# Kernel optimization log

Measured on AMD Instinct MI355X. Metric: run time of the kernel, lower is better.

## Reference

```python
import jax, jax.numpy as jnp
import numpy as np

N_NODES = 100000
N_EDGES = 6400000
F_IN, F_HID, F_OUT = 5, 5, 10


def setup_inputs() -> dict:
    key = jax.random.key(0)
    ks = jax.random.split(key, 9)
    x = jax.random.normal(ks[0], (N_NODES, F_IN), dtype=jnp.float32)
    src = jax.random.randint(ks[1], (N_EDGES,), 0, N_NODES, dtype=jnp.int32)
    dst = jax.random.randint(ks[2], (N_EDGES,), 0, N_NODES, dtype=jnp.int32)
    s1 = 1.0 / np.sqrt(F_IN)
    s2 = 1.0 / np.sqrt(F_HID)
    W_self1 = jax.random.uniform(ks[3], (F_IN, F_HID), jnp.float32, -s1, s1)
    W_neigh1 = jax.random.uniform(ks[4], (F_IN, F_HID), jnp.float32, -s1, s1)
    b1 = jnp.zeros((F_HID,), jnp.float32)
    W_self2 = jax.random.uniform(ks[5], (F_HID, F_OUT), jnp.float32, -s2, s2)
    W_neigh2 = jax.random.uniform(ks[6], (F_HID, F_OUT), jnp.float32, -s2, s2)
    b2 = jnp.zeros((F_OUT,), jnp.float32)
    return {"x": x, "src": src, "dst": dst,
            "W_self1": W_self1, "W_neigh1": W_neigh1, "b1": b1,
            "W_self2": W_self2, "W_neigh2": W_neigh2, "b2": b2}


def _sage_mean(h, src, dst, W_self, W_neigh, b):
    # DGL SAGEConv (mean): out = h @ W_self + mean_{u->v}(h_u) @ W_neigh + b
    msg = h[src]                                        # [E, F] gather
    agg = jax.ops.segment_sum(msg, dst, num_segments=N_NODES)   # [N, F]
    deg = jax.ops.segment_sum(jnp.ones((src.shape[0],), h.dtype), dst,
                              num_segments=N_NODES)     # [N]
    h_neigh = agg / jnp.maximum(deg, 1.0)[:, None]
    return h @ W_self + h_neigh @ W_neigh + b


def reference(x, src, dst, W_self1, W_neigh1, b1, W_self2, W_neigh2, b2):
    h = jax.nn.sigmoid(_sage_mean(x, src, dst, W_self1, W_neigh1, b1))
    out = jax.nn.sigmoid(_sage_mean(h, src, dst, W_self2, W_neigh2, b2))
    return out
```

## Files before the change

kernel.cpp:

```cpp
#include <hip/hip_runtime.h>
#include <hip/hip_fp16.h>
#include <math.h>


#define F_IN  5
#define F_HID 5
#define F_OUT 10

#define NBSHIFT 7
#define NPB     (1 << NBSHIFT)
#define PBLK    1024
#define CHUNK   8192
#define EPT     8
#define BSTRIDE 9216
#define SBLK    512
#define SPT     18
#define LPN2    8
#define LBLK    256

__device__ __forceinline__ float sigmoidf(float v) {
    return 1.0f / (1.0f + __expf(-v));
}

__global__ void partition(const float* __restrict__ x,
                          const int* __restrict__ src, const int* __restrict__ dst,
                          int* __restrict__ bcursor, int* __restrict__ packed,
                          uint4* __restrict__ xh, int E, int N, int NB) {
    __shared__ int cnt[PBLK], excl[PBLK], adj[PBLK];
    __shared__ int wsum[16];
    __shared__ int buf[CHUNK];
    __shared__ unsigned char dlow[CHUNK];
    int t = threadIdx.x;
    int lane = t & 63, w = t >> 6;
    if (t < NPB) {
        int v = (blockIdx.x << NBSHIFT) + t;
        if (v < N) {
            const float* xr = x + (size_t)v * 5;
            float4 a = *(const float4*)xr;
            float a4 = xr[4];
            uint4 o;
            o.x = (unsigned)__half_as_ushort(__float2half_rn(a.x)) |
                  ((unsigned)__half_as_ushort(__float2half_rn(a.y)) << 16);
            o.y = (unsigned)__half_as_ushort(__float2half_rn(a.z)) |
                  ((unsigned)__half_as_ushort(__float2half_rn(a.w)) << 16);
            o.z = (unsigned)__half_as_ushort(__float2half_rn(a4));
            o.w = 0;
            xh[v] = o;
        }
    }
    cnt[t] = 0;
    __syncthreads();
    int base = blockIdx.x * CHUNK;
    int end  = min(base + CHUNK, E);
    int sarr[EPT], darr[EPT];
    #pragma unroll
    for (int r = 0; r < 2; ++r) {
        int i = base + r * 4096 + t * 4;
        if (i + 4 <= end) {
            int4 sv = *(const int4*)(src + i);
            int4 dv = *(const int4*)(dst + i);
            sarr[r*4+0]=sv.x; sarr[r*4+1]=sv.y; sarr[r*4+2]=sv.z; sarr[r*4+3]=sv.w;
            darr[r*4+0]=dv.x; darr[r*4+1]=dv.y; darr[r*4+2]=dv.z; darr[r*4+3]=dv.w;
        } else {
            #pragma unroll
            for (int c = 0; c < 4; ++c) {
                int i2 = i + c;
                if (i2 < end) { sarr[r*4+c] = src[i2]; darr[r*4+c] = dst[i2]; }
            }
        }
    }
    int esd[EPT];
    int ebp[EPT];
    #pragma unroll
    for (int j = 0; j < EPT; ++j) {
        int i = base + (j >> 2) * 4096 + t * 4 + (j & 3);
        if (i < end) {
            int sv = sarr[j], d = darr[j];
            int b  = d >> NBSHIFT;
            int p  = atomicAdd(&cnt[b], 1);
            esd[j] = sv | ((d & (NPB - 1)) << 17);
            ebp[j] = (b << 14) | p;
        }
    }
    __syncthreads();
    int v = cnt[t];
    int incl = v;
    #pragma unroll
    for (int off = 1; off < 64; off <<= 1) {
        int u = __shfl_up(incl, off, 64);
        if (lane >= off) incl += u;
    }
    if (lane == 63) wsum[w] = incl;
    __syncthreads();
    if (t < 16) {
        int s = wsum[t];
        #pragma unroll
        for (int off = 1; off < 16; off <<= 1) {
            int u = __shfl_up(s, off, 16);
            if (t >= off) s += u;
        }
        wsum[t] = s;
    }
    __syncthreads();
    int wbase = (w > 0) ? wsum[w - 1] : 0;
    excl[t] = incl - v + wbase;
    __syncthreads();
    if (t < NB) {
        int cb = cnt[t];
        int go = cb ? atomicAdd(&bcursor[t], cb) : 0;
        adj[t] = t * BSTRIDE + go - excl[t];
    }
    __syncthreads();
    #pragma unroll
    for (int j = 0; j < EPT; ++j) {
        int i = base + (j >> 2) * 4096 + t * 4 + (j & 3);
        if (i < end) {
            int b   = ebp[j] >> 14;
            int pos = excl[b] + (ebp[j] & 0x3FFF);
            buf[pos]  = (esd[j] & 0x1FFFF) | (b << 17);
            dlow[pos] = (unsigned char)(esd[j] >> 17);
        }
    }
    __syncthreads();
    int cval = end - base;
    for (int p = t; p < cval; p += PBLK) {
        int e = buf[p];
        int b = e >> 17;
        packed[adj[b] + p] = (e & 0x1FFFF) | ((int)dlow[p] << 17);
    }
}

__global__ void __launch_bounds__(SBLK, 8)
sortagg1(const uint4* __restrict__ xh, int* __restrict__ packed,
         const int* __restrict__ bcursor,
         const float* __restrict__ Ws, const float* __restrict__ Wn,
         const float* __restrict__ bias,
         uint4* __restrict__ hp, int2* __restrict__ sd, int N) {
    __shared__ int buf[BSTRIDE];
    __shared__ int ncnt[NPB], nst[NPB];
    __shared__ int w0sum;
    int b = blockIdx.x, t = threadIdx.x;
    int s0  = b * BSTRIDE;
    int cnt = min(bcursor[b], BSTRIDE);
    if (t < NPB) ncnt[t] = 0;
    __syncthreads();
    int myv[SPT];
    #pragma unroll
    for (int r = 0; r < 4; ++r) {
        int i = r * 2048 + t * 4;
        if (i + 4 <= cnt) {
            int4 q = *(const int4*)(packed + s0 + i);
            myv[r*4+0]=q.x; myv[r*4+1]=q.y; myv[r*4+2]=q.z; myv[r*4+3]=q.w;
        } else {
            #pragma unroll
            for (int c = 0; c < 4; ++c) {
                int i2 = i + c;
                myv[r*4+c] = (i2 < cnt) ? packed[s0 + i2] : 0;
            }
        }
    }
    {
        int i = 8192 + t * 2;
        if (i + 2 <= cnt) {
            int2 q = *(const int2*)(packed + s0 + i);
            myv[16] = q.x; myv[17] = q.y;
        } else {
            myv[16] = (i     < cnt) ? packed[s0 + i]     : 0;
            myv[17] = (i + 1 < cnt) ? packed[s0 + i + 1] : 0;
        }
    }
    short myp[SPT];
    #pragma unroll
    for (int j = 0; j < SPT; ++j) {
        int i = (j < 16) ? ((j >> 2) * 2048 + t * 4 + (j & 3)) : (8192 + t * 2 + (j - 16));
        if (i < cnt) {
            myp[j] = (short)atomicAdd(&ncnt[(myv[j] >> 17) & (NPB - 1)], 1);
        }
    }
    __syncthreads();
    if (t < NPB) {
        int lane = t & 63;
        int vv = ncnt[t];
        int incl = vv;
        #pragma unroll
        for (int off = 1; off < 64; off <<= 1) {
            int u = __shfl_up(incl, off, 64);
            if (lane >= off) incl += u;
        }
        if (t == 63) w0sum = incl;
        nst[t] = incl - vv;
    }
    __syncthreads();
    if (t >= 64 && t < NPB) nst[t] += w0sum;
    __syncthreads();
    if (t < NPB) {
        int node = (b << NBSHIFT) + t;
        if (node < N) sd[node] = make_int2(s0 + nst[t], ncnt[t]);
    }
    __syncthreads();
    #pragma unroll
    for (int j = 0; j < SPT; ++j) {
        int i = (j < 16) ? ((j >> 2) * 2048 + t * 4 + (j & 3)) : (8192 + t * 2 + (j - 16));
        if (i < cnt) {
            int e = myv[j];
            buf[nst[(e >> 17) & (NPB - 1)] + (int)myp[j]] = e;
        }
    }
    __syncthreads();
    for (int i = t; i < cnt; i += SBLK)
        packed[s0 + i] = buf[i] & 0x1FFFF;
    int sub = t & 3, ln = t >> 2;
    int node = (b << NBSHIFT) + ln;
    float a0 = 0, a1 = 0, a2 = 0, a3 = 0, a4 = 0;
    int dg = 0;
    if (node < N) {
        int st = nst[ln];
        dg = ncnt[ln];
        for (int k = sub; k < dg; k += 4) {
            int u = buf[st + k] & 0x1FFFF;
            uint4 q = xh[u];
            float2 f01 = __half22float2(*(const __half2*)&q.x);
            float2 f23 = __half22float2(*(const __half2*)&q.y);
            float2 f45 = __half22float2(*(const __half2*)&q.z);
            a0 += f01.x; a1 += f01.y; a2 += f23.x; a3 += f23.y; a4 += f45.x;
        }
    }
    #pragma unroll
    for (int off = 2; off > 0; off >>= 1) {
        a0 += __shfl_down(a0, off, 4);
        a1 += __shfl_down(a1, off, 4);
        a2 += __shfl_down(a2, off, 4);
        a3 += __shfl_down(a3, off, 4);
        a4 += __shfl_down(a4, off, 4);
    }
    if (sub != 0 || node >= N) return;
    float rd = 1.0f / fmaxf((float)dg, 1.0f);
    float ni[F_IN] = { a0 * rd, a1 * rd, a2 * rd, a3 * rd, a4 * rd };
    uint4 qs = xh[node];
    float2 s01 = __half22float2(*(const __half2*)&qs.x);
    float2 s23 = __half22float2(*(const __half2*)&qs.y);
    float2 s45 = __half22float2(*(const __half2*)&qs.z);
    float xi[F_IN] = { s01.x, s01.y, s23.x, s23.y, s45.x };
    unsigned short hu[5];
    #pragma unroll
    for (int j = 0; j < F_HID; ++j) {
        float acc = bias[j];
        #pragma unroll
        for (int f = 0; f < F_IN; ++f)
            acc += xi[f] * Ws[f * F_HID + j] + ni[f] * Wn[f * F_HID + j];
        hu[j] = __half_as_ushort(__float2half_rn(sigmoidf(acc)));
    }
    uint4 o;
    o.x = (unsigned)hu[0] | ((unsigned)hu[1] << 16);
    o.y = (unsigned)hu[2] | ((unsigned)hu[3] << 16);
    o.z = (unsigned)hu[4];
    o.w = 0;
    hp[node] = o;
}

__global__ void layer2(const uint4* __restrict__ hp, const int* __restrict__ eidx,
                       const int2* __restrict__ sd,
                       const float* __restrict__ Ws, const float* __restrict__ Wn,
                       const float* __restrict__ b,
                       float* __restrict__ out, int N) {
    int tid = blockIdx.x * blockDim.x + threadIdx.x;
    int v   = tid >> 3;
    int sub = threadIdx.x & (LPN2 - 1);
    if (v >= N) return;
    int2 sdv = sd[v];
    int st = sdv.x, dg = sdv.y;
    int len = (dg + LPN2 - 1) >> 3;
    int k0 = sub * len;
    int k1 = min(k0 + len, dg);
    float s0 = 0, s1 = 0, s2 = 0, s3 = 0, s4 = 0;
    int k = k0;
    for (; k + 4 <= k1; k += 4) {
        int4 qi;
        __builtin_memcpy(&qi, eidx + st + k, 16);
        #pragma unroll
        for (int c = 0; c < 4; ++c) {
            int u = (c == 0) ? qi.x : (c == 1) ? qi.y : (c == 2) ? qi.z : qi.w;
            uint4 q = hp[u];
            float2 f01 = __half22float2(*(const __half2*)&q.x);
            float2 f23 = __half22float2(*(const __half2*)&q.y);
            float2 f45 = __half22float2(*(const __half2*)&q.z);
            s0 += f01.x; s1 += f01.y; s2 += f23.x; s3 += f23.y; s4 += f45.x;
        }
    }
    for (; k < k1; ++k) {
        int u = eidx[st + k];
        uint4 q = hp[u];
        float2 f01 = __half22float2(*(const __half2*)&q.x);
        float2 f23 = __half22float2(*(const __half2*)&q.y);
        float2 f45 = __half22float2(*(const __half2*)&q.z);
        s0 += f01.x; s1 += f01.y; s2 += f23.x; s3 += f23.y; s4 += f45.x;
    }
    #pragma unroll
    for (int off = LPN2 / 2; off > 0; off >>= 1) {
        s0 += __shfl_down(s0, off, LPN2);
        s1 += __shfl_down(s1, off, LPN2);
        s2 += __shfl_down(s2, off, LPN2);
        s3 += __shfl_down(s3, off, LPN2);
        s4 += __shfl_down(s4, off, LPN2);
    }
    if (sub != 0) return;
    float rd = 1.0f / fmaxf((float)dg, 1.0f);
    float ni[F_HID] = { s0 * rd, s1 * rd, s2 * rd, s3 * rd, s4 * rd };
    uint4 q = hp[v];
    float2 f01 = __half22float2(*(const __half2*)&q.x);
    float2 f23 = __half22float2(*(const __half2*)&q.y);
    float2 f45 = __half22float2(*(const __half2*)&q.z);
    float hi[F_HID] = { f01.x, f01.y, f23.x, f23.y, f45.x };
    #pragma unroll
    for (int j = 0; j < F_OUT; ++j) {
        float acc = b[j];
        #pragma unroll
        for (int f = 0; f < F_HID; ++f)
            acc += hi[f] * Ws[f * F_OUT + j] + ni[f] * Wn[f * F_OUT + j];
        out[(size_t)v * F_OUT + j] = sigmoidf(acc);
    }
}

extern "C" void kernel_launch(void* const* d_in, const int* in_sizes, int n_in,
                              void* d_out, int out_size, void* d_ws, size_t ws_size,
                              hipStream_t stream) {
    const float* x   = (const float*)d_in[0];
    const int*   src = (const int*)d_in[1];
    const int*   dst = (const int*)d_in[2];
    const float* Ws1 = (const float*)d_in[3];
    const float* Wn1 = (const float*)d_in[4];
    const float* b1  = (const float*)d_in[5];
    const float* Ws2 = (const float*)d_in[6];
    const float* Wn2 = (const float*)d_in[7];
    const float* b2  = (const float*)d_in[8];
    float* out = (float*)d_out;

    const int N  = in_sizes[0] / F_IN;
    const int E  = in_sizes[1];
    const int NB = (N + NPB - 1) >> NBSHIFT;

    int*   bcursor = (int*)d_ws;
    uint4* xh      = (uint4*)(bcursor + 1024);
    int2*  sd      = (int2*)(xh + N);
    int*   packed  = (int*)(sd + N);
    uint4* hp      = (uint4*)(packed + (size_t)NB * BSTRIDE);

    const int ablocks = (E + CHUNK - 1) / CHUNK;
    const int lgrid   = ((size_t)N * LPN2 + LBLK - 1) / LBLK;

    (void)hipMemsetAsync(bcursor, 0, 1024 * sizeof(int), stream);
    partition<<<ablocks, PBLK, 0, stream>>>(x, src, dst, bcursor, packed, xh, E, N, NB);
    sortagg1<<<NB, SBLK, 0, stream>>>(xh, packed, bcursor, Ws1, Wn1, b1, hp, sd, N);
    layer2<<<lgrid, LBLK, 0, stream>>>(hp, packed, sd, Ws2, Wn2, b2, out, N);
}
```

Before: 200.1 us.

## Fuse partition, sort-aggregate and layer-2 into one cooperative persistent kernel

```diff
diff --git a/kernel.cpp b/kernel.cpp
--- a/kernel.cpp
+++ b/kernel.cpp
@@ -1,6 +1,9 @@
 #include <hip/hip_runtime.h>
 #include <hip/hip_fp16.h>
+#include <hip/hip_cooperative_groups.h>
 #include <math.h>
+
+namespace cg = cooperative_groups;
 
 
 #define F_IN  5
@@ -17,9 +20,341 @@
 #define SPT     18
 #define LPN2    8
 #define LBLK    256
+#define FBLK    512
+#define EPTF    16
 
 __device__ __forceinline__ float sigmoidf(float v) {
     return 1.0f / (1.0f + __expf(-v));
+}
+
+__device__ __forceinline__ uint4 pack_h5(const float* __restrict__ xr) {
+    float4 a = *(const float4*)xr;
+    float a4 = xr[4];
+    uint4 o;
+    o.x = (unsigned)__half_as_ushort(__float2half_rn(a.x)) |
+          ((unsigned)__half_as_ushort(__float2half_rn(a.y)) << 16);
+    o.y = (unsigned)__half_as_ushort(__float2half_rn(a.z)) |
+          ((unsigned)__half_as_ushort(__float2half_rn(a.w)) << 16);
+    o.z = (unsigned)__half_as_ushort(__float2half_rn(a4));
+    o.w = 0;
+    return o;
+}
+
+union SharedU {
+    struct {
+        int cnt[1024];
+        int excl[1024];
+        int adj[1024];
+        int wsum[16];
+        int buf[CHUNK];
+        unsigned char dlow[CHUNK];
+    } part;
+    struct {
+        int buf[BSTRIDE];
+        int ncnt[NPB];
+        int nst[NPB];
+        int w0sum;
+    } srt;
+};
+
+__global__ void __launch_bounds__(FBLK, 4)
+fused(const float* __restrict__ x,
+      const int* __restrict__ src, const int* __restrict__ dst,
+      int* __restrict__ bcursor, int* __restrict__ packed,
+      uint4* __restrict__ xh,
+      const float* __restrict__ Ws1, const float* __restrict__ Wn1,
+      const float* __restrict__ b1,
+      uint4* __restrict__ hp, int2* __restrict__ sd,
+      const float* __restrict__ Ws2, const float* __restrict__ Wn2,
+      const float* __restrict__ b2,
+      float* __restrict__ out,
+      int E, int N, int NB, int NCHUNK, int NG2) {
+    __shared__ SharedU sh;
+    cg::grid_group gg = cg::this_grid();
+    int t = threadIdx.x;
+    int lane = t & 63, w = t >> 6;
+
+    if (blockIdx.x == 0) { bcursor[t] = 0; bcursor[t + FBLK] = 0; }
+    __threadfence();
+    gg.sync();
+    __threadfence();
+
+    for (int cc = blockIdx.x; cc < NCHUNK; cc += gridDim.x) {
+        int base = cc * CHUNK;
+        int end  = min(base + CHUNK, E);
+        sh.part.cnt[t] = 0;
+        sh.part.cnt[t + FBLK] = 0;
+        if (t < NPB) {
+            int v = (cc << NBSHIFT) + t;
+            if (v < N) xh[v] = pack_h5(x + (size_t)v * 5);
+        }
+        __syncthreads();
+        int sarr[EPTF], darr[EPTF];
+        #pragma unroll
+        for (int r = 0; r < 4; ++r) {
+            int i = base + r * 2048 + t * 4;
+            if (i + 4 <= end) {
+                int4 sv = *(const int4*)(src + i);
+                int4 dv = *(const int4*)(dst + i);
+                sarr[r*4+0]=sv.x; sarr[r*4+1]=sv.y; sarr[r*4+2]=sv.z; sarr[r*4+3]=sv.w;
+                darr[r*4+0]=dv.x; darr[r*4+1]=dv.y; darr[r*4+2]=dv.z; darr[r*4+3]=dv.w;
+            } else {
+                #pragma unroll
+                for (int c = 0; c < 4; ++c) {
+                    int i2 = i + c;
+                    if (i2 < end) { sarr[r*4+c] = src[i2]; darr[r*4+c] = dst[i2]; }
+                }
+            }
+        }
+        #pragma unroll
+        for (int j = 0; j < EPTF; ++j) {
+            int i = base + (j >> 2) * 2048 + t * 4 + (j & 3);
+            if (i < end) {
+                int d = darr[j];
+                int b = d >> NBSHIFT;
+                int p = atomicAdd(&sh.part.cnt[b], 1);
+                sarr[j] |= (d & (NPB - 1)) << 17;
+                darr[j] = (b << 14) | p;
+            }
+        }
+        __syncthreads();
+        int c0 = sh.part.cnt[2 * t], c1 = sh.part.cnt[2 * t + 1];
+        int s = c0 + c1;
+        int incl = s;
+        #pragma unroll
+        for (int off = 1; off < 64; off <<= 1) {
+            int u = __shfl_up(incl, off, 64);
+            if (lane >= off) incl += u;
+        }
+        if (lane == 63) sh.part.wsum[w] = incl;
+        __syncthreads();
+        if (t < 8) {
+            int sv = sh.part.wsum[t];
+            #pragma unroll
+            for (int off = 1; off < 8; off <<= 1) {
+                int u = __shfl_up(sv, off, 8);
+                if (t >= off) sv += u;
+            }
+            sh.part.wsum[t] = sv;
+        }
+        __syncthreads();
+        int wbase = (w > 0) ? sh.part.wsum[w - 1] : 0;
+        int e0 = incl - s + wbase;
+        sh.part.excl[2 * t]     = e0;
+        sh.part.excl[2 * t + 1] = e0 + c0;
+        __syncthreads();
+        for (int bb = t; bb < NB; bb += FBLK) {
+            int cb = sh.part.cnt[bb];
+            int go = cb ? atomicAdd(&bcursor[bb], cb) : 0;
+            sh.part.adj[bb] = bb * BSTRIDE + go - sh.part.excl[bb];
+        }
+        __syncthreads();
+        #pragma unroll
+        for (int j = 0; j < EPTF; ++j) {
+            int i = base + (j >> 2) * 2048 + t * 4 + (j & 3);
+            if (i < end) {
+                int b   = darr[j] >> 14;
+                int pos = sh.part.excl[b] + (darr[j] & 0x3FFF);
+                sh.part.buf[pos]  = (sarr[j] & 0x1FFFF) | (b << 17);
+                sh.part.dlow[pos] = (unsigned char)(sarr[j] >> 17);
+            }
+        }
+        __syncthreads();
+        int cval = end - base;
+        for (int p = t; p < cval; p += FBLK) {
+            int e = sh.part.buf[p];
+            int b = e >> 17;
+            packed[sh.part.adj[b] + p] = (e & 0x1FFFF) | ((int)sh.part.dlow[p] << 17);
+        }
+        __syncthreads();
+    }
+    __threadfence();
+    gg.sync();
+    __threadfence();
+
+    for (int bb = blockIdx.x; bb < NB; bb += gridDim.x) {
+        int sb   = bb * BSTRIDE;
+        int cntb = min(bcursor[bb], BSTRIDE);
+        if (t < NPB) sh.srt.ncnt[t] = 0;
+        __syncthreads();
+        int myv[SPT];
+        #pragma unroll
+        for (int r = 0; r < 4; ++r) {
+            int i = r * 2048 + t * 4;
+            if (i + 4 <= cntb) {
+                int4 q = *(const int4*)(packed + sb + i);
+                myv[r*4+0]=q.x; myv[r*4+1]=q.y; myv[r*4+2]=q.z; myv[r*4+3]=q.w;
+            } else {
+                #pragma unroll
+                for (int c = 0; c < 4; ++c) {
+                    int i2 = i + c;
+                    myv[r*4+c] = (i2 < cntb) ? packed[sb + i2] : 0;
+                }
+            }
+        }
+        {
+            int i = 8192 + t * 2;
+            if (i + 2 <= cntb) {
+                int2 q = *(const int2*)(packed + sb + i);
+                myv[16] = q.x; myv[17] = q.y;
+            } else {
+                myv[16] = (i     < cntb) ? packed[sb + i]     : 0;
+                myv[17] = (i + 1 < cntb) ? packed[sb + i + 1] : 0;
+            }
+        }
+        short myp[SPT];
+        #pragma unroll
+        for (int j = 0; j < SPT; ++j) {
+            int i = (j < 16) ? ((j >> 2) * 2048 + t * 4 + (j & 3)) : (8192 + t * 2 + (j - 16));
+            if (i < cntb) {
+                myp[j] = (short)atomicAdd(&sh.srt.ncnt[(myv[j] >> 17) & (NPB - 1)], 1);
+            }
+        }
+        __syncthreads();
+        if (t < NPB) {
+            int vv = sh.srt.ncnt[t];
+            int incl = vv;
+            #pragma unroll
+            for (int off = 1; off < 64; off <<= 1) {
+                int u = __shfl_up(incl, off, 64);
+                if ((t & 63) >= off) incl += u;
+            }
+            if (t == 63) sh.srt.w0sum = incl;
+            sh.srt.nst[t] = incl - vv;
+        }
+        __syncthreads();
+        if (t >= 64 && t < NPB) sh.srt.nst[t] += sh.srt.w0sum;
+        __syncthreads();
+        if (t < NPB) {
+            int node = (bb << NBSHIFT) + t;
+            if (node < N) sd[node] = make_int2(sb + sh.srt.nst[t], sh.srt.ncnt[t]);
+        }
+        __syncthreads();
+        #pragma unroll
+        for (int j = 0; j < SPT; ++j) {
+            int i = (j < 16) ? ((j >> 2) * 2048 + t * 4 + (j & 3)) : (8192 + t * 2 + (j - 16));
+            if (i < cntb) {
+                int e = myv[j];
+                sh.srt.buf[sh.srt.nst[(e >> 17) & (NPB - 1)] + (int)myp[j]] = e;
+            }
+        }
+        __syncthreads();
+        for (int i = t; i < cntb; i += FBLK)
+            packed[sb + i] = sh.srt.buf[i] & 0x1FFFF;
+        int sub = t & 3, ln = t >> 2;
+        int node = (bb << NBSHIFT) + ln;
+        float a0 = 0, a1 = 0, a2 = 0, a3 = 0, a4 = 0;
+        int dg = 0;
+        if (node < N) {
+            int st = sh.srt.nst[ln];
+            dg = sh.srt.ncnt[ln];
+            for (int k = sub; k < dg; k += 4) {
+                int u = sh.srt.buf[st + k] & 0x1FFFF;
+                uint4 q = xh[u];
+                float2 f01 = __half22float2(*(const __half2*)&q.x);
+                float2 f23 = __half22float2(*(const __half2*)&q.y);
+                float2 f45 = __half22float2(*(const __half2*)&q.z);
+                a0 += f01.x; a1 += f01.y; a2 += f23.x; a3 += f23.y; a4 += f45.x;
+            }
+        }
+        #pragma unroll
+        for (int off = 2; off > 0; off >>= 1) {
+            a0 += __shfl_down(a0, off, 4);
+            a1 += __shfl_down(a1, off, 4);
+            a2 += __shfl_down(a2, off, 4);
+            a3 += __shfl_down(a3, off, 4);
+            a4 += __shfl_down(a4, off, 4);
+        }
+        if (sub == 0 && node < N) {
+            float rd = 1.0f / fmaxf((float)dg, 1.0f);
+            float ni[F_IN] = { a0 * rd, a1 * rd, a2 * rd, a3 * rd, a4 * rd };
+            uint4 qs = xh[node];
+            float2 s01 = __half22float2(*(const __half2*)&qs.x);
+            float2 s23 = __half22float2(*(const __half2*)&qs.y);
+            float2 s45 = __half22float2(*(const __half2*)&qs.z);
+            float xi[F_IN] = { s01.x, s01.y, s23.x, s23.y, s45.x };
+            unsigned short hu[5];
+            #pragma unroll
+            for (int j = 0; j < F_HID; ++j) {
+                float acc = b1[j];
+                #pragma unroll
+                for (int f = 0; f < F_IN; ++f)
+                    acc += xi[f] * Ws1[f * F_HID + j] + ni[f] * Wn1[f * F_HID + j];
+                hu[j] = __half_as_ushort(__float2half_rn(sigmoidf(acc)));
+            }
+            uint4 o;
+            o.x = (unsigned)hu[0] | ((unsigned)hu[1] << 16);
+            o.y = (unsigned)hu[2] | ((unsigned)hu[3] << 16);
+            o.z = (unsigned)hu[4];
+            o.w = 0;
+            hp[node] = o;
+        }
+        __syncthreads();
+    }
+    __threadfence();
+    gg.sync();
+    __threadfence();
+
+    for (int g = blockIdx.x; g < NG2; g += gridDim.x) {
+        int v   = (g << 6) + (t >> 3);
+        int sub = t & (LPN2 - 1);
+        float s0 = 0, s1 = 0, s2 = 0, s3 = 0, s4 = 0;
+        int stv = 0, dg = 0;
+        if (v < N) {
+            int2 sdv = sd[v];
+            stv = sdv.x; dg = sdv.y;
+        }
+        int len = (dg + LPN2 - 1) >> 3;
+        int k0 = sub * len;
+        int k1 = min(k0 + len, dg);
+        int k = k0;
+        for (; k + 4 <= k1; k += 4) {
+            int4 qi;
+            __builtin_memcpy(&qi, packed + stv + k, 16);
+            #pragma unroll
+            for (int c = 0; c < 4; ++c) {
+                int u = (c == 0) ? qi.x : (c == 1) ? qi.y : (c == 2) ? qi.z : qi.w;
+                uint4 q = hp[u];
+                float2 f01 = __half22float2(*(const __half2*)&q.x);
+                float2 f23 = __half22float2(*(const __half2*)&q.y);
+                float2 f45 = __half22float2(*(const __half2*)&q.z);
+                s0 += f01.x; s1 += f01.y; s2 += f23.x; s3 += f23.y; s4 += f45.x;
+            }
+        }
+        for (; k < k1; ++k) {
+            int u = packed[stv + k];
+            uint4 q = hp[u];
+            float2 f01 = __half22float2(*(const __half2*)&q.x);
+            float2 f23 = __half22float2(*(const __half2*)&q.y);
+            float2 f45 = __half22float2(*(const __half2*)&q.z);
+            s0 += f01.x; s1 += f01.y; s2 += f23.x; s3 += f23.y; s4 += f45.x;
+        }
+        #pragma unroll
+        for (int off = LPN2 / 2; off > 0; off >>= 1) {
+            s0 += __shfl_down(s0, off, LPN2);
+            s1 += __shfl_down(s1, off, LPN2);
+            s2 += __shfl_down(s2, off, LPN2);
+            s3 += __shfl_down(s3, off, LPN2);
+            s4 += __shfl_down(s4, off, LPN2);
+        }
+        if (sub == 0 && v < N) {
+            float rd = 1.0f / fmaxf((float)dg, 1.0f);
+            float ni[F_HID] = { s0 * rd, s1 * rd, s2 * rd, s3 * rd, s4 * rd };
+            uint4 q = hp[v];
+            float2 f01 = __half22float2(*(const __half2*)&q.x);
+            float2 f23 = __half22float2(*(const __half2*)&q.y);
+            float2 f45 = __half22float2(*(const __half2*)&q.z);
+            float hi[F_HID] = { f01.x, f01.y, f23.x, f23.y, f45.x };
+            #pragma unroll
+            for (int j = 0; j < F_OUT; ++j) {
+                float acc = b2[j];
+                #pragma unroll
+                for (int f = 0; f < F_HID; ++f)
+                    acc += hi[f] * Ws2[f * F_OUT + j] + ni[f] * Wn2[f * F_OUT + j];
+                out[(size_t)v * F_OUT + j] = sigmoidf(acc);
+            }
+        }
+    }
 }
 
 __global__ void partition(const float* __restrict__ x,
@@ -34,19 +369,7 @@
     int lane = t & 63, w = t >> 6;
     if (t < NPB) {
         int v = (blockIdx.x << NBSHIFT) + t;
-        if (v < N) {
-            const float* xr = x + (size_t)v * 5;
-            float4 a = *(const float4*)xr;
-            float a4 = xr[4];
-            uint4 o;
-            o.x = (unsigned)__half_as_ushort(__float2half_rn(a.x)) |
-                  ((unsigned)__half_as_ushort(__float2half_rn(a.y)) << 16);
-            o.y = (unsigned)__half_as_ushort(__float2half_rn(a.z)) |
-                  ((unsigned)__half_as_ushort(__float2half_rn(a.w)) << 16);
-            o.z = (unsigned)__half_as_ushort(__float2half_rn(a4));
-            o.w = 0;
-            xh[v] = o;
-        }
+        if (v < N) xh[v] = pack_h5(x + (size_t)v * 5);
     }
     cnt[t] = 0;
     __syncthreads();
@@ -69,8 +392,7 @@
             }
         }
     }
-    int esd[EPT];
-    int ebp[EPT];
+    int esd[EPT], ebp[EPT];
     #pragma unroll
     for (int j = 0; j < EPT; ++j) {
         int i = base + (j >> 2) * 4096 + t * 4 + (j & 3);
@@ -338,6 +660,8 @@
     const int N  = in_sizes[0] / F_IN;
     const int E  = in_sizes[1];
     const int NB = (N + NPB - 1) >> NBSHIFT;
+    const int NCHUNK = (E + CHUNK - 1) / CHUNK;
+    const int NG2 = (N + 63) >> 6;
 
     int*   bcursor = (int*)d_ws;
     uint4* xh      = (uint4*)(bcursor + 1024);
@@ -345,6 +669,32 @@
     int*   packed  = (int*)(sd + N);
     uint4* hp      = (uint4*)(packed + (size_t)NB * BSTRIDE);
 
+    static int coop_blocks = -2;
+    if (coop_blocks == -2) {
+        int dev = 0; (void)hipGetDevice(&dev);
+        int can = 0, ncu = 0, bpc = 0;
+        (void)hipDeviceGetAttribute(&can, hipDeviceAttributeCooperativeLaunch, dev);
+        (void)hipDeviceGetAttribute(&ncu, hipDeviceAttributeMultiprocessorCount, dev);
+        hipError_t oe = hipOccupancyMaxActiveBlocksPerMultiprocessor(&bpc, fused, FBLK, 0);
+        coop_blocks = (can && ncu > 0 && oe == hipSuccess && bpc > 0) ? bpc * ncu : 0;
+    }
+
+    if (coop_blocks > 0) {
+        int grid = coop_blocks;
+        if (grid > NG2) grid = NG2;
+        int e_ = E, n_ = N, nb_ = NB, nc_ = NCHUNK, ng_ = NG2;
+        void* args[] = {
+            (void*)&x, (void*)&src, (void*)&dst, (void*)&bcursor, (void*)&packed,
+            (void*)&xh, (void*)&Ws1, (void*)&Wn1, (void*)&b1, (void*)&hp, (void*)&sd,
+            (void*)&Ws2, (void*)&Wn2, (void*)&b2, (void*)&out,
+            (void*)&e_, (void*)&n_, (void*)&nb_, (void*)&nc_, (void*)&ng_
+        };
+        hipError_t err = hipLaunchCooperativeKernel((const void*)fused, dim3(grid),
+                                                    dim3(FBLK), args, 0, stream);
+        if (err == hipSuccess) return;
+        coop_blocks = 0;
+    }
+
     const int ablocks = (E + CHUNK - 1) / CHUNK;
     const int lgrid   = ((size_t)N * LPN2 + LBLK - 1) / LBLK;
 
```

New measurement: 521.6 us. 2.61x slower.

## Replace per-node sort with shared-memory atomic accumulation per bucket

Applied to the files above, without the earlier changes.

```diff
diff --git a/kernel.cpp b/kernel.cpp
--- a/kernel.cpp
+++ b/kernel.cpp
@@ -13,13 +13,31 @@
 #define CHUNK   8192
 #define EPT     8
 #define BSTRIDE 9216
-#define SBLK    512
-#define SPT     18
-#define LPN2    8
-#define LBLK    256
+#define ABLK    256
+#define REP     2
 
 __device__ __forceinline__ float sigmoidf(float v) {
     return 1.0f / (1.0f + __expf(-v));
+}
+
+__device__ __forceinline__ uint4 pack_h5(const float* __restrict__ xr) {
+    float4 a = *(const float4*)xr;
+    float a4 = xr[4];
+    uint4 o;
+    o.x = (unsigned)__half_as_ushort(__float2half_rn(a.x)) |
+          ((unsigned)__half_as_ushort(__float2half_rn(a.y)) << 16);
+    o.y = (unsigned)__half_as_ushort(__float2half_rn(a.z)) |
+          ((unsigned)__half_as_ushort(__float2half_rn(a.w)) << 16);
+    o.z = (unsigned)__half_as_ushort(__float2half_rn(a4));
+    o.w = 0;
+    return o;
+}
+
+__device__ __forceinline__ void unp5(uint4 q, float* f) {
+    float2 f01 = __half22float2(*(const __half2*)&q.x);
+    float2 f23 = __half22float2(*(const __half2*)&q.y);
+    float2 f45 = __half22float2(*(const __half2*)&q.z);
+    f[0] = f01.x; f[1] = f01.y; f[2] = f23.x; f[3] = f23.y; f[4] = f45.x;
 }
 
 __global__ void partition(const float* __restrict__ x,
@@ -34,19 +52,7 @@
     int lane = t & 63, w = t >> 6;
     if (t < NPB) {
         int v = (blockIdx.x << NBSHIFT) + t;
-        if (v < N) {
-            const float* xr = x + (size_t)v * 5;
-            float4 a = *(const float4*)xr;
-            float a4 = xr[4];
-            uint4 o;
-            o.x = (unsigned)__half_as_ushort(__float2half_rn(a.x)) |
-                  ((unsigned)__half_as_ushort(__float2half_rn(a.y)) << 16);
-            o.y = (unsigned)__half_as_ushort(__float2half_rn(a.z)) |
-                  ((unsigned)__half_as_ushort(__float2half_rn(a.w)) << 16);
-            o.z = (unsigned)__half_as_ushort(__float2half_rn(a4));
-            o.w = 0;
-            xh[v] = o;
-        }
+        if (v < N) xh[v] = pack_h5(x + (size_t)v * 5);
     }
     cnt[t] = 0;
     __syncthreads();
@@ -130,194 +136,171 @@
     }
 }
 
-__global__ void __launch_bounds__(SBLK, 8)
-sortagg1(const uint4* __restrict__ xh, int* __restrict__ packed,
-         const int* __restrict__ bcursor,
-         const float* __restrict__ Ws, const float* __restrict__ Wn,
-         const float* __restrict__ bias,
-         uint4* __restrict__ hp, int2* __restrict__ sd, int N) {
-    __shared__ int buf[BSTRIDE];
-    __shared__ int ncnt[NPB], nst[NPB];
-    __shared__ int w0sum;
+__global__ void __launch_bounds__(ABLK, 4)
+agg1(const uint4* __restrict__ xh, const int* __restrict__ packed,
+     const int* __restrict__ bcursor,
+     const float* __restrict__ Ws, const float* __restrict__ Wn,
+     const float* __restrict__ bias,
+     uint4* __restrict__ hp, float* __restrict__ rdeg, int N) {
+    __shared__ float accf[REP * NPB * F_IN];
+    __shared__ int ncnt[NPB];
     int b = blockIdx.x, t = threadIdx.x;
     int s0  = b * BSTRIDE;
     int cnt = min(bcursor[b], BSTRIDE);
+    for (int i = t; i < REP * NPB * F_IN; i += ABLK) accf[i] = 0.0f;
     if (t < NPB) ncnt[t] = 0;
     __syncthreads();
-    int myv[SPT];
-    #pragma unroll
-    for (int r = 0; r < 4; ++r) {
-        int i = r * 2048 + t * 4;
+    int rep = t & (REP - 1);
+    for (int i = t * 4; i < cnt; i += ABLK * 4) {
         if (i + 4 <= cnt) {
             int4 q = *(const int4*)(packed + s0 + i);
-            myv[r*4+0]=q.x; myv[r*4+1]=q.y; myv[r*4+2]=q.z; myv[r*4+3]=q.w;
+            int e0 = q.x, e1 = q.y, e2 = q.z, e3 = q.w;
+            uint4 g0 = xh[e0 & 0x1FFFF];
+            uint4 g1 = xh[e1 & 0x1FFFF];
+            uint4 g2 = xh[e2 & 0x1FFFF];
+            uint4 g3 = xh[e3 & 0x1FFFF];
+            int n0 = (e0 >> 17) & (NPB - 1);
+            int n1 = (e1 >> 17) & (NPB - 1);
+            int n2 = (e2 >> 17) & (NPB - 1);
+            int n3 = (e3 >> 17) & (NPB - 1);
+            float f[F_IN];
+            float* a;
+            unp5(g0, f); a = accf + (rep * NPB + n0) * F_IN;
+            atomicAdd(a+0,f[0]); atomicAdd(a+1,f[1]); atomicAdd(a+2,f[2]);
+            atomicAdd(a+3,f[3]); atomicAdd(a+4,f[4]); atomicAdd(&ncnt[n0],1);
+            unp5(g1, f); a = accf + (rep * NPB + n1) * F_IN;
+            atomicAdd(a+0,f[0]); atomicAdd(a+1,f[1]); atomicAdd(a+2,f[2]);
+            atomicAdd(a+3,f[3]); atomicAdd(a+4,f[4]); atomicAdd(&ncnt[n1],1);
+            unp5(g2, f); a = accf + (rep * NPB + n2) * F_IN;
+            atomicAdd(a+0,f[0]); atomicAdd(a+1,f[1]); atomicAdd(a+2,f[2]);
+            atomicAdd(a+3,f[3]); atomicAdd(a+4,f[4]); atomicAdd(&ncnt[n2],1);
+            unp5(g3, f); a = accf + (rep * NPB + n3) * F_IN;
+            atomicAdd(a+0,f[0]); atomicAdd(a+1,f[1]); atomicAdd(a+2,f[2]);
+            atomicAdd(a+3,f[3]); atomicAdd(a+4,f[4]); atomicAdd(&ncnt[n3],1);
         } else {
-            #pragma unroll
             for (int c = 0; c < 4; ++c) {
-                int i2 = i + c;
-                myv[r*4+c] = (i2 < cnt) ? packed[s0 + i2] : 0;
-            }
-        }
-    }
-    {
-        int i = 8192 + t * 2;
-        if (i + 2 <= cnt) {
-            int2 q = *(const int2*)(packed + s0 + i);
-            myv[16] = q.x; myv[17] = q.y;
-        } else {
-            myv[16] = (i     < cnt) ? packed[s0 + i]     : 0;
-            myv[17] = (i + 1 < cnt) ? packed[s0 + i + 1] : 0;
-        }
-    }
-    short myp[SPT];
-    #pragma unroll
-    for (int j = 0; j < SPT; ++j) {
-        int i = (j < 16) ? ((j >> 2) * 2048 + t * 4 + (j & 3)) : (8192 + t * 2 + (j - 16));
-        if (i < cnt) {
-            myp[j] = (short)atomicAdd(&ncnt[(myv[j] >> 17) & (NPB - 1)], 1);
-        }
-    }
-    __syncthreads();
-    if (t < NPB) {
-        int lane = t & 63;
-        int vv = ncnt[t];
-        int incl = vv;
-        #pragma unroll
-        for (int off = 1; off < 64; off <<= 1) {
-            int u = __shfl_up(incl, off, 64);
-            if (lane >= off) incl += u;
-        }
-        if (t == 63) w0sum = incl;
-        nst[t] = incl - vv;
-    }
-    __syncthreads();
-    if (t >= 64 && t < NPB) nst[t] += w0sum;
+                if (i + c < cnt) {
+                    int e = packed[s0 + i + c];
+                    int n = (e >> 17) & (NPB - 1);
+                    float f[F_IN];
+                    unp5(xh[e & 0x1FFFF], f);
+                    float* a = accf + (rep * NPB + n) * F_IN;
+                    atomicAdd(a+0,f[0]); atomicAdd(a+1,f[1]); atomicAdd(a+2,f[2]);
+                    atomicAdd(a+3,f[3]); atomicAdd(a+4,f[4]); atomicAdd(&ncnt[n],1);
+                }
+            }
+        }
+    }
     __syncthreads();
     if (t < NPB) {
         int node = (b << NBSHIFT) + t;
-        if (node < N) sd[node] = make_int2(s0 + nst[t], ncnt[t]);
-    }
-    __syncthreads();
-    #pragma unroll
-    for (int j = 0; j < SPT; ++j) {
-        int i = (j < 16) ? ((j >> 2) * 2048 + t * 4 + (j & 3)) : (8192 + t * 2 + (j - 16));
-        if (i < cnt) {
-            int e = myv[j];
-            buf[nst[(e >> 17) & (NPB - 1)] + (int)myp[j]] = e;
-        }
-    }
-    __syncthreads();
-    for (int i = t; i < cnt; i += SBLK)
-        packed[s0 + i] = buf[i] & 0x1FFFF;
-    int sub = t & 3, ln = t >> 2;
-    int node = (b << NBSHIFT) + ln;
-    float a0 = 0, a1 = 0, a2 = 0, a3 = 0, a4 = 0;
-    int dg = 0;
-    if (node < N) {
-        int st = nst[ln];
-        dg = ncnt[ln];
-        for (int k = sub; k < dg; k += 4) {
-            int u = buf[st + k] & 0x1FFFF;
-            uint4 q = xh[u];
-            float2 f01 = __half22float2(*(const __half2*)&q.x);
-            float2 f23 = __half22float2(*(const __half2*)&q.y);
-            float2 f45 = __half22float2(*(const __half2*)&q.z);
-            a0 += f01.x; a1 += f01.y; a2 += f23.x; a3 += f23.y; a4 += f45.x;
-        }
-    }
-    #pragma unroll
-    for (int off = 2; off > 0; off >>= 1) {
-        a0 += __shfl_down(a0, off, 4);
-        a1 += __shfl_down(a1, off, 4);
-        a2 += __shfl_down(a2, off, 4);
-        a3 += __shfl_down(a3, off, 4);
-        a4 += __shfl_down(a4, off, 4);
-    }
-    if (sub != 0 || node >= N) return;
-    float rd = 1.0f / fmaxf((float)dg, 1.0f);
-    float ni[F_IN] = { a0 * rd, a1 * rd, a2 * rd, a3 * rd, a4 * rd };
-    uint4 qs = xh[node];
-    float2 s01 = __half22float2(*(const __half2*)&qs.x);
-    float2 s23 = __half22float2(*(const __half2*)&qs.y);
-    float2 s45 = __half22float2(*(const __half2*)&qs.z);
-    float xi[F_IN] = { s01.x, s01.y, s23.x, s23.y, s45.x };
-    unsigned short hu[5];
-    #pragma unroll
-    for (int j = 0; j < F_HID; ++j) {
-        float acc = bias[j];
-        #pragma unroll
-        for (int f = 0; f < F_IN; ++f)
-            acc += xi[f] * Ws[f * F_HID + j] + ni[f] * Wn[f * F_HID + j];
-        hu[j] = __half_as_ushort(__float2half_rn(sigmoidf(acc)));
-    }
-    uint4 o;
-    o.x = (unsigned)hu[0] | ((unsigned)hu[1] << 16);
-    o.y = (unsigned)hu[2] | ((unsigned)hu[3] << 16);
-    o.z = (unsigned)hu[4];
-    o.w = 0;
-    hp[node] = o;
-}
-
-__global__ void layer2(const uint4* __restrict__ hp, const int* __restrict__ eidx,
-                       const int2* __restrict__ sd,
-                       const float* __restrict__ Ws, const float* __restrict__ Wn,
-                       const float* __restrict__ b,
-                       float* __restrict__ out, int N) {
-    int tid = blockIdx.x * blockDim.x + threadIdx.x;
-    int v   = tid >> 3;
-    int sub = threadIdx.x & (LPN2 - 1);
-    if (v >= N) return;
-    int2 sdv = sd[v];
-    int st = sdv.x, dg = sdv.y;
-    int len = (dg + LPN2 - 1) >> 3;
-    int k0 = sub * len;
-    int k1 = min(k0 + len, dg);
-    float s0 = 0, s1 = 0, s2 = 0, s3 = 0, s4 = 0;
-    int k = k0;
-    for (; k + 4 <= k1; k += 4) {
-        int4 qi;
-        __builtin_memcpy(&qi, eidx + st + k, 16);
-        #pragma unroll
-        for (int c = 0; c < 4; ++c) {
-            int u = (c == 0) ? qi.x : (c == 1) ? qi.y : (c == 2) ? qi.z : qi.w;
-            uint4 q = hp[u];
-            float2 f01 = __half22float2(*(const __half2*)&q.x);
-            float2 f23 = __half22float2(*(const __half2*)&q.y);
-            float2 f45 = __half22float2(*(const __half2*)&q.z);
-            s0 += f01.x; s1 += f01.y; s2 += f23.x; s3 += f23.y; s4 += f45.x;
-        }
-    }
-    for (; k < k1; ++k) {
-        int u = eidx[st + k];
-        uint4 q = hp[u];
-        float2 f01 = __half22float2(*(const __half2*)&q.x);
-        float2 f23 = __half22float2(*(const __half2*)&q.y);
-        float2 f45 = __half22float2(*(const __half2*)&q.z);
-        s0 += f01.x; s1 += f01.y; s2 += f23.x; s3 += f23.y; s4 += f45.x;
-    }
-    #pragma unroll
-    for (int off = LPN2 / 2; off > 0; off >>= 1) {
-        s0 += __shfl_down(s0, off, LPN2);
-        s1 += __shfl_down(s1, off, LPN2);
-        s2 += __shfl_down(s2, off, LPN2);
-        s3 += __shfl_down(s3, off, LPN2);
-        s4 += __shfl_down(s4, off, LPN2);
-    }
-    if (sub != 0) return;
-    float rd = 1.0f / fmaxf((float)dg, 1.0f);
-    float ni[F_HID] = { s0 * rd, s1 * rd, s2 * rd, s3 * rd, s4 * rd };
-    uint4 q = hp[v];
-    float2 f01 = __half22float2(*(const __half2*)&q.x);
-    float2 f23 = __half22float2(*(const __half2*)&q.y);
-    float2 f45 = __half22float2(*(const __half2*)&q.z);
-    float hi[F_HID] = { f01.x, f01.y, f23.x, f23.y, f45.x };
-    #pragma unroll
-    for (int j = 0; j < F_OUT; ++j) {
-        float acc = b[j];
-        #pragma unroll
-        for (int f = 0; f < F_HID; ++f)
-            acc += hi[f] * Ws[f * F_OUT + j] + ni[f] * Wn[f * F_OUT + j];
-        out[(size_t)v * F_OUT + j] = sigmoidf(acc);
+        if (node < N) {
+            int dg = ncnt[t];
+            float rd = 1.0f / fmaxf((float)dg, 1.0f);
+            float ni[F_IN];
+            #pragma unroll
+            for (int f = 0; f < F_IN; ++f)
+                ni[f] = (accf[t * F_IN + f] + accf[(NPB + t) * F_IN + f]) * rd;
+            float xi[F_IN];
+            unp5(xh[node], xi);
+            unsigned short hu[F_HID];
+            #pragma unroll
+            for (int j = 0; j < F_HID; ++j) {
+                float acc = bias[j];
+                #pragma unroll
+                for (int f = 0; f < F_IN; ++f)
+                    acc += xi[f] * Ws[f * F_HID + j] + ni[f] * Wn[f * F_HID + j];
+                hu[j] = __half_as_ushort(__float2half_rn(sigmoidf(acc)));
+            }
+            uint4 o;
+            o.x = (unsigned)hu[0] | ((unsigned)hu[1] << 16);
+            o.y = (unsigned)hu[2] | ((unsigned)hu[3] << 16);
+            o.z = (unsigned)hu[4];
+            o.w = 0;
+            hp[node] = o;
+            rdeg[node] = rd;
+        }
+    }
+}
+
+__global__ void __launch_bounds__(ABLK, 4)
+agg2(const uint4* __restrict__ hp, const int* __restrict__ packed,
+     const int* __restrict__ bcursor, const float* __restrict__ rdeg,
+     const float* __restrict__ Ws, const float* __restrict__ Wn,
+     const float* __restrict__ bias,
+     float* __restrict__ out, int N) {
+    __shared__ float accf[REP * NPB * F_HID];
+    int b = blockIdx.x, t = threadIdx.x;
+    int s0  = b * BSTRIDE;
+    int cnt = min(bcursor[b], BSTRIDE);
+    for (int i = t; i < REP * NPB * F_HID; i += ABLK) accf[i] = 0.0f;
+    __syncthreads();
+    int rep = t & (REP - 1);
+    for (int i = t * 4; i < cnt; i += ABLK * 4) {
+        if (i + 4 <= cnt) {
+            int4 q = *(const int4*)(packed + s0 + i);
+            int e0 = q.x, e1 = q.y, e2 = q.z, e3 = q.w;
+            uint4 g0 = hp[e0 & 0x1FFFF];
+            uint4 g1 = hp[e1 & 0x1FFFF];
+            uint4 g2 = hp[e2 & 0x1FFFF];
+            uint4 g3 = hp[e3 & 0x1FFFF];
+            int n0 = (e0 >> 17) & (NPB - 1);
+            int n1 = (e1 >> 17) & (NPB - 1);
+            int n2 = (e2 >> 17) & (NPB - 1);
+            int n3 = (e3 >> 17) & (NPB - 1);
+            float f[F_HID];
+            float* a;
+            unp5(g0, f); a = accf + (rep * NPB + n0) * F_HID;
+            atomicAdd(a+0,f[0]); atomicAdd(a+1,f[1]); atomicAdd(a+2,f[2]);
+            atomicAdd(a+3,f[3]); atomicAdd(a+4,f[4]);
+            unp5(g1, f); a = accf + (rep * NPB + n1) * F_HID;
+            atomicAdd(a+0,f[0]); atomicAdd(a+1,f[1]); atomicAdd(a+2,f[2]);
+            atomicAdd(a+3,f[3]); atomicAdd(a+4,f[4]);
+            unp5(g2, f); a = accf + (rep * NPB + n2) * F_HID;
+            atomicAdd(a+0,f[0]); atomicAdd(a+1,f[1]); atomicAdd(a+2,f[2]);
+            atomicAdd(a+3,f[3]); atomicAdd(a+4,f[4]);
+            unp5(g3, f); a = accf + (rep * NPB + n3) * F_HID;
+            atomicAdd(a+0,f[0]); atomicAdd(a+1,f[1]); atomicAdd(a+2,f[2]);
+            atomicAdd(a+3,f[3]); atomicAdd(a+4,f[4]);
+        } else {
+            for (int c = 0; c < 4; ++c) {
+                if (i + c < cnt) {
+                    int e = packed[s0 + i + c];
+                    int n = (e >> 17) & (NPB - 1);
+                    float f[F_HID];
+                    unp5(hp[e & 0x1FFFF], f);
+                    float* a = accf + (rep * NPB + n) * F_HID;
+                    atomicAdd(a+0,f[0]); atomicAdd(a+1,f[1]); atomicAdd(a+2,f[2]);
+                    atomicAdd(a+3,f[3]); atomicAdd(a+4,f[4]);
+                }
+            }
+        }
+    }
+    __syncthreads();
+    if (t < NPB) {
+        int node = (b << NBSHIFT) + t;
+        if (node < N) {
+            float rd = rdeg[node];
+            float ni[F_HID];
+            #pragma unroll
+            for (int f = 0; f < F_HID; ++f)
+                ni[f] = (accf[t * F_HID + f] + accf[(NPB + t) * F_HID + f]) * rd;
+            float hi[F_HID];
+            unp5(hp[node], hi);
+            float o[F_OUT];
+            #pragma unroll
+            for (int j = 0; j < F_OUT; ++j) {
+                float acc = bias[j];
+                #pragma unroll
+                for (int f = 0; f < F_HID; ++f)
+                    acc += hi[f] * Ws[f * F_OUT + j] + ni[f] * Wn[f * F_OUT + j];
+                o[j] = sigmoidf(acc);
+            }
+            float* op = out + (size_t)node * F_OUT;
+            #pragma unroll
+            for (int j = 0; j < F_OUT; j += 2)
+                *(float2*)(op + j) = make_float2(o[j], o[j + 1]);
+        }
     }
 }
 
@@ -341,15 +324,14 @@
 
     int*   bcursor = (int*)d_ws;
     uint4* xh      = (uint4*)(bcursor + 1024);
-    int2*  sd      = (int2*)(xh + N);
-    int*   packed  = (int*)(sd + N);
+    float* rdeg    = (float*)(xh + N);
+    int*   packed  = (int*)(rdeg + N);
     uint4* hp      = (uint4*)(packed + (size_t)NB * BSTRIDE);
 
     const int ablocks = (E + CHUNK - 1) / CHUNK;
-    const int lgrid   = ((size_t)N * LPN2 + LBLK - 1) / LBLK;
 
     (void)hipMemsetAsync(bcursor, 0, 1024 * sizeof(int), stream);
     partition<<<ablocks, PBLK, 0, stream>>>(x, src, dst, bcursor, packed, xh, E, N, NB);
-    sortagg1<<<NB, SBLK, 0, stream>>>(xh, packed, bcursor, Ws1, Wn1, b1, hp, sd, N);
-    layer2<<<lgrid, LBLK, 0, stream>>>(hp, packed, sd, Ws2, Wn2, b2, out, N);
-}
+    agg1<<<NB, ABLK, 0, stream>>>(xh, packed, bcursor, Ws1, Wn1, b1, hp, rdeg, N);
+    agg2<<<NB, ABLK, 0, stream>>>(hp, packed, bcursor, rdeg, Ws2, Wn2, b2, out, N);
+}
```

Result: slower. 551.1 us (+175.4%).
